# Kernel tuning notes

Measured on AMD Instinct MI355X. Metric: run time of the kernel, lower is better.

The kernel has to match this reference:

```python
import jax, jax.numpy as jnp
import numpy as np

DIM = 512
HEADS = 8
SCALE = (DIM // HEADS) ** -0.5  # 0.125
B, H, W = 1, 64, 64  # square spatial grid required by torch matmul broadcasting


def setup_inputs() -> dict:
    key = jax.random.key(0)
    ks = jax.random.split(key, 7)
    s = DIM ** -0.5
    return {
        "x": jax.random.normal(ks[0], (B, H, W, DIM), dtype=jnp.float32),
        "mask": 0,  # sentinel for None (mask must be None in the original)
        "Wq": jax.random.normal(ks[1], (DIM, DIM), dtype=jnp.float32) * s,
        "bq": jax.random.normal(ks[2], (DIM,), dtype=jnp.float32) * 0.01,
        "Wk": jax.random.normal(ks[3], (DIM, DIM), dtype=jnp.float32) * s,
        "bk": jax.random.normal(ks[4], (DIM,), dtype=jnp.float32) * 0.01,
        "Wv": jax.random.normal(ks[5], (DIM, DIM), dtype=jnp.float32) * s,
        "bv": jax.random.normal(ks[6], (DIM,), dtype=jnp.float32) * 0.01,
    }


def reference(x, mask, Wq, bq, Wk, bk, Wv, bv):
    # Linear projections (nn.Linear: x @ W.T + b)
    q = jnp.einsum('bhwc,oc->bhwo', x, Wq) + bq
    k = jnp.einsum('bhwc,oc->bhwo', x, Wk) + bk
    v = jnp.einsum('bhwc,oc->bhwo', x, Wv) + bv
    # Faithful to torch.einsum('bhwc,bpqd->bhwpq', q, k): c and d are each
    # summed independently => outer product of channel-sums. [b,h,w,p,q]
    weights = jnp.einsum('bhwc,bpqd->bhwpq', q, k)
    # dropout is identity in eval mode; then scale and softmax over last axis
    weights = jax.nn.softmax(weights * SCALE, axis=-1)
    # torch matmul broadcasting: [b,h,w,p,q] @ [b,p,q,d] -> [b,h,w,p,d]
    attn = jnp.matmul(weights, v)
    return attn
```

## Files before the change

kernel.cpp:

```cpp
#include <hip/hip_runtime.h>

typedef _Float16 half8 __attribute__((ext_vector_type(8)));
typedef float f32x4 __attribute__((ext_vector_type(4)));
typedef float float4_t __attribute__((ext_vector_type(4)));
typedef unsigned int uint32x2 __attribute__((ext_vector_type(2)));

#define DIM 512
#define S 64
#define NROW 4096
#define LDSW 88

__device__ __forceinline__ void bar_lds() {
    asm volatile("s_waitcnt lgkmcnt(0)" ::: "memory");
    __builtin_amdgcn_s_barrier();
    asm volatile("" ::: "memory");
}

__global__ void colsum2_kernel(const float* __restrict__ Wq, const float* __restrict__ bq,
                               const float* __restrict__ Wk, const float* __restrict__ bk,
                               float* __restrict__ wsumq, float* __restrict__ wsumk) {
    int sel = blockIdx.x >> 7;
    int b = blockIdx.x & 127;
    const float* W = sel ? Wk : Wq;
    const float* bias = sel ? bk : bq;
    float* wsum = sel ? wsumk : wsumq;
    int t = threadIdx.x;
    int c0 = t, c1 = t + 256;
    float s0 = 0.f, s1 = 0.f;
    const float* Wr = W + (size_t)b * 4 * DIM;
#pragma unroll
    for (int o = 0; o < 4; ++o) {
        s0 += Wr[o * DIM + c0];
        s1 += Wr[o * DIM + c1];
    }
    atomicAdd(&wsum[c0], s0);
    atomicAdd(&wsum[c1], s1);
    if (b == 0) {
        float bs = bias[c0] + bias[c1];
#pragma unroll
        for (int off = 32; off >= 1; off >>= 1) bs += __shfl_xor(bs, off);
        if ((t & 63) == 0) atomicAdd(&wsum[512], bs);
    }
}

__global__ void rowdot_vt_kernel(const float* __restrict__ X,
                                 const float* __restrict__ wqsum,
                                 const float* __restrict__ wksum,
                                 float* __restrict__ a_arr,
                                 float* __restrict__ ks_arr,
                                 const float* __restrict__ Wv,
                                 const float* __restrict__ bv,
                                 _Float16* __restrict__ Vs) {
    int bid = blockIdx.x;
    if (bid < 1024) {
        int wave = threadIdx.x >> 6;
        int lane = threadIdx.x & 63;
        int row = bid * 4 + wave;
        const float4_t* xr = (const float4_t*)(X + (size_t)row * DIM) + lane * 2;
        const float4_t* wq = (const float4_t*)wqsum + lane * 2;
        const float4_t* wk = (const float4_t*)wksum + lane * 2;
        float4_t x0 = xr[0], x1 = xr[1];
        float4_t q0 = wq[0], q1 = wq[1];
        float4_t k0 = wk[0], k1 = wk[1];
        float sq = 0.f, sk = 0.f;
#pragma unroll
        for (int i = 0; i < 4; i++) {
            sq += x0[i] * q0[i] + x1[i] * q1[i];
            sk += x0[i] * k0[i] + x1[i] * k1[i];
        }
#pragma unroll
        for (int off = 32; off >= 1; off >>= 1) {
            sq += __shfl_xor(sq, off);
            sk += __shfl_xor(sk, off);
        }
        if (lane == 0) {
            a_arr[row]  = (sq + wqsum[DIM]) * 0.125f;
            ks_arr[row] = sk + wksum[DIM];
        }
        return;
    }
    int b2 = bid - 1024;
    int mb = b2 & 255;
    int cb = b2 >> 8;
    int wv_ = threadIdx.x >> 6;
    int lane = threadIdx.x & 63;
    int lr = lane & 15;
    int lg = lane >> 4;
    int row0 = mb * 16;
    int col0 = cb * 256 + wv_ * 64;

    f32x4 acc[4];
#pragma unroll
    for (int n = 0; n < 4; n++) acc[n] = (f32x4){0.f, 0.f, 0.f, 0.f};

    for (int kk = 0; kk < 16; ++kk) {
        int kbase = kk * 32 + lg * 8;
        const float4_t* pa = (const float4_t*)(X + (size_t)(row0 + lr) * DIM + kbase);
        float4_t x0 = pa[0], x1 = pa[1];
        half8 a;
#pragma unroll
        for (int i = 0; i < 4; i++) { a[i] = (_Float16)x0[i]; a[i + 4] = (_Float16)x1[i]; }
#pragma unroll
        for (int n = 0; n < 4; n++) {
            const float4_t* pb = (const float4_t*)(Wv + (size_t)(col0 + n * 16 + lr) * DIM + kbase);
            float4_t b0 = pb[0], b1 = pb[1];
            half8 hb;
#pragma unroll
            for (int i = 0; i < 4; i++) { hb[i] = (_Float16)b0[i]; hb[i + 4] = (_Float16)b1[i]; }
            acc[n] = __builtin_amdgcn_mfma_f32_16x16x32_f16(a, hb, acc[n], 0, 0, 0);
        }
    }
    int w   = mb >> 2;
    int s_  = (mb & 3) >> 1;
    int lg2 = ((mb & 3) * 2 + (lg >> 1)) & 3;
    int e0  = (lg & 1) * 4;
#pragma unroll
    for (int n = 0; n < 4; n++) {
        int d = col0 + n * 16 + lr;
        int dt = d >> 4;
        float bvc = bv[d];
        _Float16 tmp[4];
#pragma unroll
        for (int r = 0; r < 4; r++) tmp[r] = (_Float16)(acc[n][r] + bvc);
        int idx8 = (((w * 32 + dt) * 2 + s_) * 4 + lg2) * 16 + lr;
        __builtin_nontemporal_store(*(uint32x2*)tmp, (uint32x2*)(Vs + (size_t)idx8 * 8 + e0));
    }
}

__global__ __launch_bounds__(256) void attn_main_kernel(
        const float* __restrict__ a_arr,
        const float* __restrict__ ks_arr,
        const _Float16* __restrict__ Vs,
        float* __restrict__ out) {
    __shared__ __align__(16) char smem[32768];
    _Float16* Wsm = (_Float16*)smem;
    char* Osm = smem;

    int b = blockIdx.x;
    int l = (b & 7) * 256 + (b >> 3);
    int w = l >> 5;
    int h0 = (l & 31) * 2;
    int t = threadIdx.x;
    int wv_ = t >> 6, lane = t & 63;
    int lr = lane & 15, lg = lane >> 4;

    const half8* Vg = (const half8*)Vs;

    half8 vfr[4][2][2];
#pragma unroll
    for (int j2 = 0; j2 < 4; ++j2)
#pragma unroll
        for (int c = 0; c < 2; ++c) {
            int dt = j2 * 8 + wv_ * 2 + c;
            int g0 = ((w * 32 + dt) * 2) * 64 + lane;
            vfr[j2][c][0] = Vg[g0];
            vfr[j2][c][1] = Vg[g0 + 64];
        }

    float a0 = a_arr[h0 * 64 + w];
    float a1 = a_arr[(h0 + 1) * 64 + w];

    for (int hh = 0; hh < 2; ++hh) {
        float a = hh ? a1 : a0;
        int hw = (h0 + hh) * 64 + w;

        bar_lds();

        {
            int p = t >> 2, c = t & 3;
            const float4_t* kp = (const float4_t*)(ks_arr + p * 64 + c * 16);
            float4_t k0 = kp[0], k1 = kp[1], k2 = kp[2], k3 = kp[3];
            float L[16];
#pragma unroll
            for (int i = 0; i < 4; i++) {
                L[i] = a * k0[i]; L[4 + i] = a * k1[i];
                L[8 + i] = a * k2[i]; L[12 + i] = a * k3[i];
            }
            float m = L[0];
#pragma unroll
            for (int i = 1; i < 16; i++) m = fmaxf(m, L[i]);
            m = fmaxf(m, __shfl_xor(m, 1));
            m = fmaxf(m, __shfl_xor(m, 2));
            float e[16];
            float sum = 0.f;
#pragma unroll
            for (int i = 0; i < 16; i++) { e[i] = __expf(L[i] - m); sum += e[i]; }
            sum += __shfl_xor(sum, 1);
            sum += __shfl_xor(sum, 2);
            float r = 1.0f / sum;
            half8 hv0, hv1;
#pragma unroll
            for (int i = 0; i < 8; i++) {
                hv0[i] = (_Float16)(e[i] * r);
                hv1[i] = (_Float16)(e[8 + i] * r);
            }
            *(half8*)&Wsm[p * LDSW + c * 16]     = hv0;
            *(half8*)&Wsm[p * LDSW + c * 16 + 8] = hv1;
        }
        bar_lds();

        half8 wfr[4][2];
#pragma unroll
        for (int pt = 0; pt < 4; ++pt)
#pragma unroll
            for (int s_ = 0; s_ < 2; ++s_)
                wfr[pt][s_] = *(const half8*)&Wsm[(pt * 16 + lr) * LDSW + s_ * 32 + lg * 8];

        char* outb = (char*)(out + (size_t)hw * (64 * DIM));

#pragma unroll
        for (int j2 = 0; j2 < 4; ++j2) {
            f32x4 acc[2][4];
#pragma unroll
            for (int c = 0; c < 2; ++c)
#pragma unroll
                for (int pt = 0; pt < 4; ++pt) acc[c][pt] = (f32x4){0.f, 0.f, 0.f, 0.f};
#pragma unroll
            for (int pt = 0; pt < 4; ++pt) {
                acc[0][pt] = __builtin_amdgcn_mfma_f32_16x16x32_f16(vfr[j2][0][0], wfr[pt][0], acc[0][pt], 0, 0, 0);
                acc[0][pt] = __builtin_amdgcn_mfma_f32_16x16x32_f16(vfr[j2][0][1], wfr[pt][1], acc[0][pt], 0, 0, 0);
                acc[1][pt] = __builtin_amdgcn_mfma_f32_16x16x32_f16(vfr[j2][1][0], wfr[pt][0], acc[1][pt], 0, 0, 0);
                acc[1][pt] = __builtin_amdgcn_mfma_f32_16x16x32_f16(vfr[j2][1][1], wfr[pt][1], acc[1][pt], 0, 0, 0);
            }
            bar_lds();
#pragma unroll
            for (int c = 0; c < 2; ++c)
#pragma unroll
                for (int pt = 0; pt < 4; ++pt) {
                    int p = pt * 16 + lr;
                    int addr = p * 512 + (wv_ * 32 + c * 16 + lg * 4) * 4;
                    addr ^= (p & 7) << 4;
                    *(f32x4*)(Osm + addr) = acc[c][pt];
                }
            bar_lds();
#pragma unroll
            for (int i = 0; i < 8; ++i) {
                int f = i * 4096 + t * 16;
                int row = f >> 9;
                int rb = f ^ ((row & 7) << 4);
                f32x4 val = *(const f32x4*)(Osm + rb);
                __builtin_nontemporal_store(val, (f32x4*)(outb + (size_t)row * 2048 + j2 * 512 + (f & 511)));
            }
        }
    }
}

extern "C" void kernel_launch(void* const* d_in, const int* in_sizes, int n_in,
                              void* d_out, int out_size, void* d_ws, size_t ws_size,
                              hipStream_t stream) {
    const float* x  = (const float*)d_in[0];
    const float* Wq = (const float*)d_in[2];
    const float* bq = (const float*)d_in[3];
    const float* Wk = (const float*)d_in[4];
    const float* bk = (const float*)d_in[5];
    const float* Wv = (const float*)d_in[6];
    const float* bv = (const float*)d_in[7];
    float* out = (float*)d_out;
    char* ws = (char*)d_ws;

    _Float16* Vs  = (_Float16*)ws;
    float* a_arr  = (float*)(ws + 4194304);
    float* ks_arr = (float*)(ws + 4210688);
    float* wqsum  = (float*)(ws + 4227072);
    float* wksum  = (float*)(ws + 4229184);

    hipMemsetAsync(ws + 4227072, 0, 4224, stream);
    colsum2_kernel<<<256, 256, 0, stream>>>(Wq, bq, Wk, bk, wqsum, wksum);
    rowdot_vt_kernel<<<1536, 256, 0, stream>>>(x, wqsum, wksum, a_arr, ks_arr, Wv, bv, Vs);
    attn_main_kernel<<<2048, 256, 0, stream>>>(a_arr, ks_arr, Vs, out);
}
```

Measured before the change: 145.9 us.

## Merge column-sum into V-projection kernel and drop memset and atomics

Removes the memset and atomic-based column-sum kernel. The Wq/Wk column sums now run as 8 blocks inside the V-projection kernel, each writing partial sums with plain stores. A separate rowdot kernel then combines the 4 partials per matrix. Launch count stays at 3 but the memset disappears. The cost is that each of the 8 column-sum blocks loops over 128 rows serially, which could make those blocks stragglers within the V kernel.

```diff
diff --git a/kernel.cpp b/kernel.cpp
--- a/kernel.cpp
+++ b/kernel.cpp
@@ -16,70 +16,41 @@
     asm volatile("" ::: "memory");
 }
 
-__global__ void colsum2_kernel(const float* __restrict__ Wq, const float* __restrict__ bq,
-                               const float* __restrict__ Wk, const float* __restrict__ bk,
-                               float* __restrict__ wsumq, float* __restrict__ wsumk) {
-    int sel = blockIdx.x >> 7;
-    int b = blockIdx.x & 127;
-    const float* W = sel ? Wk : Wq;
-    const float* bias = sel ? bk : bq;
-    float* wsum = sel ? wsumk : wsumq;
-    int t = threadIdx.x;
-    int c0 = t, c1 = t + 256;
-    float s0 = 0.f, s1 = 0.f;
-    const float* Wr = W + (size_t)b * 4 * DIM;
-#pragma unroll
-    for (int o = 0; o < 4; ++o) {
-        s0 += Wr[o * DIM + c0];
-        s1 += Wr[o * DIM + c1];
-    }
-    atomicAdd(&wsum[c0], s0);
-    atomicAdd(&wsum[c1], s1);
-    if (b == 0) {
-        float bs = bias[c0] + bias[c1];
-#pragma unroll
-        for (int off = 32; off >= 1; off >>= 1) bs += __shfl_xor(bs, off);
-        if ((t & 63) == 0) atomicAdd(&wsum[512], bs);
-    }
-}
-
-__global__ void rowdot_vt_kernel(const float* __restrict__ X,
-                                 const float* __restrict__ wqsum,
-                                 const float* __restrict__ wksum,
-                                 float* __restrict__ a_arr,
-                                 float* __restrict__ ks_arr,
+__global__ void colsum_vt_kernel(const float* __restrict__ Wq, const float* __restrict__ bq,
+                                 const float* __restrict__ Wk, const float* __restrict__ bk,
+                                 float* __restrict__ part,
+                                 float* __restrict__ pbias,
+                                 const float* __restrict__ X,
                                  const float* __restrict__ Wv,
                                  const float* __restrict__ bv,
                                  _Float16* __restrict__ Vs) {
     int bid = blockIdx.x;
-    if (bid < 1024) {
-        int wave = threadIdx.x >> 6;
-        int lane = threadIdx.x & 63;
-        int row = bid * 4 + wave;
-        const float4_t* xr = (const float4_t*)(X + (size_t)row * DIM) + lane * 2;
-        const float4_t* wq = (const float4_t*)wqsum + lane * 2;
-        const float4_t* wk = (const float4_t*)wksum + lane * 2;
-        float4_t x0 = xr[0], x1 = xr[1];
-        float4_t q0 = wq[0], q1 = wq[1];
-        float4_t k0 = wk[0], k1 = wk[1];
-        float sq = 0.f, sk = 0.f;
-#pragma unroll
-        for (int i = 0; i < 4; i++) {
-            sq += x0[i] * q0[i] + x1[i] * q1[i];
-            sk += x0[i] * k0[i] + x1[i] * k1[i];
-        }
-#pragma unroll
-        for (int off = 32; off >= 1; off >>= 1) {
-            sq += __shfl_xor(sq, off);
-            sk += __shfl_xor(sk, off);
-        }
-        if (lane == 0) {
-            a_arr[row]  = (sq + wqsum[DIM]) * 0.125f;
-            ks_arr[row] = sk + wksum[DIM];
+    if (bid < 8) {
+        int sel = bid >> 2, qr = bid & 3;
+        const float* W = sel ? Wk : Wq;
+        const float* bias = sel ? bk : bq;
+        int t = threadIdx.x;
+        int c0 = t, c1 = t + 256;
+        float s0 = 0.f, s1 = 0.f;
+        const float* Wr = W + (size_t)qr * 128 * DIM;
+        for (int o = 0; o < 128; ++o) {
+            s0 += Wr[o * DIM + c0];
+            s1 += Wr[o * DIM + c1];
+        }
+        part[(sel * 4 + qr) * 512 + c0] = s0;
+        part[(sel * 4 + qr) * 512 + c1] = s1;
+        if (qr == 0) {
+            float bs = bias[c0] + bias[c1];
+#pragma unroll
+            for (int off = 32; off >= 1; off >>= 1) bs += __shfl_xor(bs, off);
+            __shared__ float red[4];
+            if ((t & 63) == 0) red[t >> 6] = bs;
+            __syncthreads();
+            if (t == 0) pbias[sel] = red[0] + red[1] + red[2] + red[3];
         }
         return;
     }
-    int b2 = bid - 1024;
+    int b2 = bid - 8;
     int mb = b2 & 255;
     int cb = b2 >> 8;
     int wv_ = threadIdx.x >> 6;
@@ -124,6 +95,40 @@
         for (int r = 0; r < 4; r++) tmp[r] = (_Float16)(acc[n][r] + bvc);
         int idx8 = (((w * 32 + dt) * 2 + s_) * 4 + lg2) * 16 + lr;
         __builtin_nontemporal_store(*(uint32x2*)tmp, (uint32x2*)(Vs + (size_t)idx8 * 8 + e0));
+    }
+}
+
+__global__ void rowdot_kernel(const float* __restrict__ X,
+                              const float* __restrict__ part,
+                              const float* __restrict__ pbias,
+                              float* __restrict__ a_arr,
+                              float* __restrict__ ks_arr) {
+    int wave = threadIdx.x >> 6;
+    int lane = threadIdx.x & 63;
+    int row = blockIdx.x * 4 + wave;
+    const float4_t* xr = (const float4_t*)(X + (size_t)row * DIM) + lane * 2;
+    float4_t x0 = xr[0], x1 = xr[1];
+    float sq = 0.f, sk = 0.f;
+#pragma unroll
+    for (int qr = 0; qr < 4; ++qr) {
+        const float4_t* pq = (const float4_t*)(part + qr * 512) + lane * 2;
+        const float4_t* pk = (const float4_t*)(part + 2048 + qr * 512) + lane * 2;
+        float4_t q0 = pq[0], q1 = pq[1];
+        float4_t k0 = pk[0], k1 = pk[1];
+#pragma unroll
+        for (int i = 0; i < 4; i++) {
+            sq += x0[i] * q0[i] + x1[i] * q1[i];
+            sk += x0[i] * k0[i] + x1[i] * k1[i];
+        }
+    }
+#pragma unroll
+    for (int off = 32; off >= 1; off >>= 1) {
+        sq += __shfl_xor(sq, off);
+        sk += __shfl_xor(sk, off);
+    }
+    if (lane == 0) {
+        a_arr[row]  = (sq + pbias[0]) * 0.125f;
+        ks_arr[row] = sk + pbias[1];
     }
 }
 
@@ -261,11 +266,10 @@
     _Float16* Vs  = (_Float16*)ws;
     float* a_arr  = (float*)(ws + 4194304);
     float* ks_arr = (float*)(ws + 4210688);
-    float* wqsum  = (float*)(ws + 4227072);
-    float* wksum  = (float*)(ws + 4229184);
-
-    hipMemsetAsync(ws + 4227072, 0, 4224, stream);
-    colsum2_kernel<<<256, 256, 0, stream>>>(Wq, bq, Wk, bk, wqsum, wksum);
-    rowdot_vt_kernel<<<1536, 256, 0, stream>>>(x, wqsum, wksum, a_arr, ks_arr, Wv, bv, Vs);
+    float* part   = (float*)(ws + 4227072);
+    float* pbias  = (float*)(ws + 4243456);
+
+    colsum_vt_kernel<<<520, 256, 0, stream>>>(Wq, bq, Wk, bk, part, pbias, x, Wv, bv, Vs);
+    rowdot_kernel<<<1024, 256, 0, stream>>>(x, part, pbias, a_arr, ks_arr);
     attn_main_kernel<<<2048, 256, 0, stream>>>(a_arr, ks_arr, Vs, out);
 }
```

Measured after the change: 139.9 us (median of 3 runs). 4.1% less time.
